# Optimization experiments

Hardware: AMD Instinct MI355X
Metric: run time of the kernel (lower is better)

## Reference

```python
import jax, jax.numpy as jnp
import numpy as np

EPS = 1e-5

@jax.custom_vjp
def spike(u):
    return (u >= 0).astype(u.dtype)

def _spike_fwd(u):
    return spike(u), u

def _spike_bwd(u, g):
    return (g / (1.0 + 5.0 * jnp.abs(u)) ** 2,)

spike.defvjp(_spike_fwd, _spike_bwd)


def setup_inputs() -> dict:
    key = jax.random.key(0)
    ks = jax.random.split(key, 20)
    B, T, IN, TH, H = 2048, 320, 64, 128, 64
    d = {}
    d['x'] = jax.random.normal(ks[0], (B, T, IN), jnp.float32)
    d['tda'] = jax.random.normal(ks[1], (B, 150), jnp.float32)
    # depthwise conv: Conv1d(64,128,k=15,pad=7,groups=64) -> kernel [128, 1, 15]
    d['conv_w'] = jax.random.normal(ks[2], (TH, 1, 15), jnp.float32) * 0.1
    d['conv_b'] = jnp.zeros((TH,), jnp.float32)
    d['bn1_g'] = jnp.ones((TH,), jnp.float32)
    d['bn1_b'] = jnp.zeros((TH,), jnp.float32)
    d['bn1_m'] = jnp.zeros((TH,), jnp.float32)
    d['bn1_v'] = jnp.ones((TH,), jnp.float32)
    # spatial_fc: Linear(128,64), init mean=0.05 std=0.1
    d['sp_w'] = 0.05 + 0.1 * jax.random.normal(ks[3], (H, TH), jnp.float32)
    d['sp_b'] = jnp.zeros((H,), jnp.float32)
    d['li_w'] = jax.random.normal(ks[4], (H, 2 * H), jnp.float32) * (1.0 / np.sqrt(2 * H))
    d['li_b'] = jnp.zeros((H,), jnp.float32)
    d['tda_w1'] = jax.random.normal(ks[5], (64, 150), jnp.float32) * (1.0 / np.sqrt(150))
    d['tda_b1'] = jnp.zeros((64,), jnp.float32)
    d['tda_w2'] = jax.random.normal(ks[6], (32, 64), jnp.float32) * 0.125
    d['tda_b2'] = jnp.zeros((32,), jnp.float32)
    dp_out = (320 // 32) * H  # 640
    d['cls_w1'] = jax.random.normal(ks[7], (128, dp_out + 32), jnp.float32) * (1.0 / np.sqrt(dp_out + 32))
    d['cls_b1'] = jnp.zeros((128,), jnp.float32)
    d['bn2_g'] = jnp.ones((128,), jnp.float32)
    d['bn2_b'] = jnp.zeros((128,), jnp.float32)
    d['bn2_m'] = jnp.zeros((128,), jnp.float32)
    d['bn2_v'] = jnp.ones((128,), jnp.float32)
    d['cls_w2'] = jax.random.normal(ks[8], (4, 128), jnp.float32) * (1.0 / np.sqrt(128))
    d['cls_b2'] = jnp.zeros((4,), jnp.float32)
    return d


def reference(x, tda, conv_w, conv_b, bn1_g, bn1_b, bn1_m, bn1_v, sp_w, sp_b,
              li_w, li_b, tda_w1, tda_b1, tda_w2, tda_b2,
              cls_w1, cls_b1, bn2_g, bn2_b, bn2_m, bn2_v, cls_w2, cls_b2):
    B, T, _ = x.shape
    L_DP, N_DP, H = 32, 16, 64
    # temp_conv (eval mode: no dropout, BN with running stats)
    xc = jnp.transpose(x, (0, 2, 1))  # [B, 64, T]
    y = jax.lax.conv_general_dilated(
        xc, conv_w, window_strides=(1,), padding=[(7, 7)],
        dimension_numbers=('NCH', 'OIH', 'NCH'), feature_group_count=64)
    y = y + conv_b[None, :, None]
    y = (y - bn1_m[None, :, None]) * jax.lax.rsqrt(bn1_v + EPS)[None, :, None] * bn1_g[None, :, None] + bn1_b[None, :, None]
    y = jax.nn.relu(y)
    y = jnp.transpose(y, (0, 2, 1))  # [B, T, 128]
    # precompute all input currents: [T, B, 64] (time-major for scan)
    cur_all = jnp.einsum('bth,oh->tbo', y, sp_w) + sp_b

    def step(carry, cur):
        mf, ms, ml = carry
        mf = 0.5 * mf + cur
        sf = spike(mf - 0.5)
        mf = mf * (1.0 - sf)
        ms = 0.9 * ms + cur
        ss = spike(ms - 1.0)
        ms = ms * (1.0 - ss)
        cur_li = jnp.concatenate([sf, ss], axis=-1) @ li_w.T + li_b
        ml = 0.9 * ml + cur_li
        return (mf, ms, ml), ml

    z0 = jnp.zeros((B, H), x.dtype)
    _, li_seq = jax.lax.scan(step, (z0, z0, z0), cur_all)  # [T, B, 64]
    li_seq = jnp.transpose(li_seq, (1, 0, 2))  # [B, T, 64]

    windows = li_seq.reshape(B, T // L_DP, L_DP, H)
    start_mean = windows[:, :, :N_DP, :].mean(axis=2)
    end_mean = windows[:, :, -N_DP:, :].mean(axis=2)
    dp_feat = (end_mean - start_mean).reshape(B, -1)  # [B, 640]

    t1 = jax.nn.relu(tda @ tda_w1.T + tda_b1)
    tda_feat = jax.nn.relu(t1 @ tda_w2.T + tda_b2)  # [B, 32]

    h = jnp.concatenate([dp_feat, tda_feat], axis=-1) @ cls_w1.T + cls_b1
    h = (h - bn2_m) * jax.lax.rsqrt(bn2_v + EPS) * bn2_g + bn2_b
    h = jax.nn.relu(h)
    return h @ cls_w2.T + cls_b2  # [B, 4]
```

## Files before the change

### kernel.cpp

```cpp
#include <hip/hip_runtime.h>

#define NT 256

#define WS_SPWT    0
#define WS_SC1     8192
#define WS_SH1     8320
#define WS_SC2     8448
#define WS_SH2     8576
#define WS_LIWT    8704
#define WS_TW1T    16896
#define WS_TW2T    26496
#define WS_CW1T    28544
#define WS_TOTAL   114560
#define WS_WG      114560
#define WS_WBASE   114688
#define WS_CURBASE (114688 + 2048*1280)
#define CUR_STRIDE 20480

__global__ void prep_kernel(
    const float* __restrict__ conv_b, const float* __restrict__ bn1_g,
    const float* __restrict__ bn1_b,  const float* __restrict__ bn1_m,
    const float* __restrict__ bn1_v,  const float* __restrict__ sp_w,
    const float* __restrict__ li_w,   const float* __restrict__ tda_w1,
    const float* __restrict__ tda_w2, const float* __restrict__ cls_w1,
    const float* __restrict__ bn2_g,  const float* __restrict__ bn2_b,
    const float* __restrict__ bn2_m,  const float* __restrict__ bn2_v,
    float* __restrict__ ws)
{
    int i = blockIdx.x * NT + threadIdx.x;
    if (i > WS_TOTAL) return;
    if (i == WS_TOTAL) {
        float g = 0.f, sE = 0.f, sL = 0.f; int w = 0;
        for (int t = 0; t < 320; ++t) {
            g = fmaf(0.9f, g, 1.f);
            int pos = t & 31;
            if (pos < 16) sE += g; else sL += g;
            if (pos == 31) { ws[WS_WG + w] = sL - sE; ++w; sE = 0.f; sL = 0.f; }
        }
        return;
    }
    if (i < WS_SC1) {
        int c = i >> 6, h = i & 63;
        ws[i] = sp_w[h*128 + c];
    } else if (i < WS_SH1) {
        int c = i - WS_SC1;
        float vv = bn1_v[c] + 1e-5f;
        ws[i] = (float)((double)bn1_g[c] / sqrt((double)vv));
    } else if (i < WS_SC2) {
        int c = i - WS_SH1;
        float vv = bn1_v[c] + 1e-5f;
        double s = (double)bn1_g[c] / sqrt((double)vv);
        ws[i] = (float)(((double)conv_b[c] - (double)bn1_m[c])*s + (double)bn1_b[c]);
    } else if (i < WS_SH2) {
        int c = i - WS_SC2;
        float vv = bn2_v[c] + 1e-5f;
        ws[i] = (float)((double)bn2_g[c] / sqrt((double)vv));
    } else if (i < WS_LIWT) {
        int c = i - WS_SH2;
        float vv = bn2_v[c] + 1e-5f;
        double s = (double)bn2_g[c] / sqrt((double)vv);
        ws[i] = (float)((double)bn2_b[c] - (double)bn2_m[c]*s);
    } else if (i < WS_TW1T) {
        int t = i - WS_LIWT; int j = t >> 6, o = t & 63;
        ws[i] = li_w[o*128 + j];
    } else if (i < WS_TW2T) {
        int t = i - WS_TW1T; int r = t >> 6, o = t & 63;
        ws[i] = tda_w1[o*150 + r];
    } else if (i < WS_CW1T) {
        int t = i - WS_TW2T; int j = t >> 5, o = t & 31;
        ws[i] = tda_w2[o*64 + j];
    } else {
        int t = i - WS_CW1T; int j = t >> 7, c = t & 127;
        ws[i] = cls_w1[c*672 + j];
    }
}

__launch_bounds__(NT, 3)
__global__ void convproj_kernel(
    const float* __restrict__ x, const float* __restrict__ conv_w,
    const float* __restrict__ ws, float* __restrict__ cur, int b0)
{
    __shared__ float smem[13312];
    float* x_lds = smem;
    float* y_lds = smem + 4992;

    const int tid  = threadIdx.x;
    const int bi   = blockIdx.x / 5;
    const int chk  = blockIdx.x % 5;
    const int b    = b0 + bi;
    const int lane = tid & 63;
    const int t0   = chk * 64;

    const int cc   = tid & 127;
    const int half = tid >> 7;
    float cwr[15];
    #pragma unroll
    for (int k = 0; k < 15; ++k) cwr[k] = conv_w[cc*15 + k];
    const float sc1 = ws[WS_SC1 + cc];
    const float sh1 = ws[WS_SH1 + cc];

    const int h0 = __builtin_amdgcn_readfirstlane((tid >> 6) << 4);
    const float* __restrict__ spwT = ws;
    const float* xb = x + (size_t)b * 20480;

    for (int idx = tid; idx < 78*16; idx += NT) {
        int trow = idx >> 4, icq = idx & 15;
        int t = t0 - 7 + trow;
        float4 v = make_float4(0.f, 0.f, 0.f, 0.f);
        if (t >= 0 && t < 320)
            v = *reinterpret_cast<const float4*>(xb + t*64 + icq*4);
        *reinterpret_cast<float4*>(&x_lds[trow*64 + icq*4]) = v;
    }
    __syncthreads();
    {
        float xr[46];
        #pragma unroll
        for (int r = 0; r < 46; ++r)
            xr[r] = x_lds[(half*32 + r)*64 + (cc >> 1)];
        #pragma unroll
        for (int i = 0; i < 32; ++i) {
            float acc = 0.f;
            #pragma unroll
            for (int k = 0; k < 15; ++k)
                acc = fmaf(xr[i + k], cwr[k], acc);
            y_lds[cc*65 + half*32 + i] = fmaxf(fmaf(acc, sc1, sh1), 0.f);
        }
    }
    __syncthreads();
    {
        float acc[16];
        #pragma unroll
        for (int j = 0; j < 16; ++j) acc[j] = 0.f;
        #pragma unroll 4
        for (int c = 0; c < 128; ++c) {
            float yv = y_lds[c*65 + lane];
            const float4* wp = reinterpret_cast<const float4*>(spwT + c*64 + h0);
            float4 w0 = wp[0], w1 = wp[1], w2 = wp[2], w3 = wp[3];
            acc[0]  = fmaf(yv, w0.x, acc[0]);
            acc[1]  = fmaf(yv, w0.y, acc[1]);
            acc[2]  = fmaf(yv, w0.z, acc[2]);
            acc[3]  = fmaf(yv, w0.w, acc[3]);
            acc[4]  = fmaf(yv, w1.x, acc[4]);
            acc[5]  = fmaf(yv, w1.y, acc[5]);
            acc[6]  = fmaf(yv, w1.z, acc[6]);
            acc[7]  = fmaf(yv, w1.w, acc[7]);
            acc[8]  = fmaf(yv, w2.x, acc[8]);
            acc[9]  = fmaf(yv, w2.y, acc[9]);
            acc[10] = fmaf(yv, w2.z, acc[10]);
            acc[11] = fmaf(yv, w2.w, acc[11]);
            acc[12] = fmaf(yv, w3.x, acc[12]);
            acc[13] = fmaf(yv, w3.y, acc[13]);
            acc[14] = fmaf(yv, w3.z, acc[14]);
            acc[15] = fmaf(yv, w3.w, acc[15]);
        }
        float* cb = cur + (size_t)bi * CUR_STRIDE + (size_t)h0 * 320 + t0 + lane;
        #pragma unroll
        for (int j = 0; j < 16; ++j)
            cb[j*320] = acc[j];
    }
}

__global__ void scan_kernel(const float* __restrict__ cur,
                            const float* __restrict__ sp_b,
                            float* __restrict__ W, int b0, int nb)
{
    const int wv = (int)((blockIdx.x * (unsigned)blockDim.x + threadIdx.x) >> 6);
    if (wv >= nb) return;
    const int lane = threadIdx.x & 63;
    const float* cb = cur + (size_t)wv * CUR_STRIDE + (size_t)lane * 320;
    const float spb = sp_b[lane];
    float* Wb = W + (size_t)(b0 + wv) * 1280;

    float mf = 0.f, ms = 0.f, rlo = 0.f, rhi = 0.f;
    float4 n0 = *reinterpret_cast<const float4*>(cb);
    float4 n1 = *reinterpret_cast<const float4*>(cb + 4);
    float4 n2 = *reinterpret_cast<const float4*>(cb + 8);
    float4 n3 = *reinterpret_cast<const float4*>(cb + 12);
    float sE_lo = 0.f, sE_hi = 0.f;

    #pragma unroll 1
    for (int tb = 0; tb < 20; ++tb) {
        float v[16];
        v[0]=n0.x; v[1]=n0.y; v[2]=n0.z; v[3]=n0.w;
        v[4]=n1.x; v[5]=n1.y; v[6]=n1.z; v[7]=n1.w;
        v[8]=n2.x; v[9]=n2.y; v[10]=n2.z; v[11]=n2.w;
        v[12]=n3.x; v[13]=n3.y; v[14]=n3.z; v[15]=n3.w;
        if (tb < 19) {
            const float* p = cb + (tb + 1) * 16;
            n0 = *reinterpret_cast<const float4*>(p);
            n1 = *reinterpret_cast<const float4*>(p + 4);
            n2 = *reinterpret_cast<const float4*>(p + 8);
            n3 = *reinterpret_cast<const float4*>(p + 12);
        }
        float slo = 0.f, shi = 0.f;
        #pragma unroll
        for (int q = 0; q < 16; ++q) {
            float c = v[q] + spb;
            mf = fmaf(0.5f, mf, c);
            bool sf = (mf - 0.5f) >= 0.f;
            ms = fmaf(0.9f, ms, c);
            bool ss = (ms - 1.0f) >= 0.f;
            mf = sf ? 0.f : mf;
            ms = ss ? 0.f : ms;
            rlo = fmaf(0.9f, rlo, sf ? 1.f : 0.f);
            rhi = fmaf(0.9f, rhi, ss ? 1.f : 0.f);
            slo += rlo; shi += rhi;
        }
        if ((tb & 1) == 0) {
            sE_lo = slo; sE_hi = shi;
        } else {
            int w = tb >> 1;
            Wb[w*128 + lane]      = slo - sE_lo;
            Wb[w*128 + 64 + lane] = shi - sE_hi;
        }
    }
}

__global__ void epilogue_kernel(
    const float* __restrict__ tda,    const float* __restrict__ li_b,
    const float* __restrict__ tda_b1, const float* __restrict__ tda_b2,
    const float* __restrict__ cls_b1, const float* __restrict__ cls_w2,
    const float* __restrict__ cls_b2, const float* __restrict__ ws,
    const float* __restrict__ W,      float* __restrict__ out)
{
    __shared__ float Wl[1280];
    __shared__ float t1[64], tf[32], dp[640], h1[128];
    const int b = blockIdx.x, tid = threadIdx.x;

    for (int i = tid; i < 1280; i += NT)
        Wl[i] = W[(size_t)b*1280 + i];
    __syncthreads();

    const float* __restrict__ liwT = ws + WS_LIWT;
    const float* __restrict__ tw1T = ws + WS_TW1T;
    const float* __restrict__ tw2T = ws + WS_TW2T;
    const float* __restrict__ cw1T = ws + WS_CW1T;
    const float* tdab = tda + b*150;

    if (tid < 64) {
        float acc = tda_b1[tid];
        for (int i2 = 0; i2 < 150; ++i2)
            acc = fmaf(tdab[i2], tw1T[i2*64 + tid], acc);
        t1[tid] = fmaxf(acc, 0.f);
    }
    __syncthreads();
    if (tid < 32) {
        float acc = tda_b2[tid];
        #pragma unroll 8
        for (int j = 0; j < 64; ++j)
            acc = fmaf(t1[j], tw2T[j*32 + tid], acc);
        tf[tid] = fmaxf(acc, 0.f);
    }
    {
        int o = tid & 63;
        for (int w = tid >> 6; w < 10; w += 4) {
            float acc = li_b[o] * ws[WS_WG + w];
            #pragma unroll 4
            for (int j = 0; j < 128; ++j)
                acc = fmaf(Wl[w*128 + j], liwT[j*64 + o], acc);
            dp[w*64 + o] = 0.0625f * acc;
        }
    }
    __syncthreads();
    if (tid < 128) {
        float acc = cls_b1[tid];
        for (int j = 0; j < 640; ++j)
            acc = fmaf(dp[j], cw1T[j*128 + tid], acc);
        #pragma unroll 4
        for (int j = 0; j < 32; ++j)
            acc = fmaf(tf[j], cw1T[(640 + j)*128 + tid], acc);
        float s2 = ws[WS_SC2 + tid], sh2 = ws[WS_SH2 + tid];
        h1[tid] = fmaxf(fmaf(acc, s2, sh2), 0.f);
    }
    __syncthreads();
    if (tid < 4) {
        float acc = cls_b2[tid];
        for (int c = 0; c < 128; ++c)
            acc = fmaf(h1[c], cls_w2[tid*128 + c], acc);
        out[b*4 + tid] = acc;
    }
}

extern "C" void kernel_launch(void* const* d_in, const int* in_sizes, int n_in,
                              void* d_out, int out_size, void* d_ws, size_t ws_size,
                              hipStream_t stream) {
    const float* x      = (const float*)d_in[0];
    const float* tda    = (const float*)d_in[1];
    const float* conv_w = (const float*)d_in[2];
    const float* conv_b = (const float*)d_in[3];
    const float* bn1_g  = (const float*)d_in[4];
    const float* bn1_b  = (const float*)d_in[5];
    const float* bn1_m  = (const float*)d_in[6];
    const float* bn1_v  = (const float*)d_in[7];
    const float* sp_w   = (const float*)d_in[8];
    const float* sp_b   = (const float*)d_in[9];
    const float* li_w   = (const float*)d_in[10];
    const float* li_b   = (const float*)d_in[11];
    const float* tda_w1 = (const float*)d_in[12];
    const float* tda_b1 = (const float*)d_in[13];
    const float* tda_w2 = (const float*)d_in[14];
    const float* tda_b2 = (const float*)d_in[15];
    const float* cls_w1 = (const float*)d_in[16];
    const float* cls_b1 = (const float*)d_in[17];
    const float* bn2_g  = (const float*)d_in[18];
    const float* bn2_b  = (const float*)d_in[19];
    const float* bn2_m  = (const float*)d_in[20];
    const float* bn2_v  = (const float*)d_in[21];
    const float* cls_w2 = (const float*)d_in[22];
    const float* cls_b2 = (const float*)d_in[23];
    float* ws  = (float*)d_ws;
    float* out = (float*)d_out;

    const int B = in_sizes[0] / (320 * 64);

    prep_kernel<<<(WS_TOTAL + 1 + NT - 1)/NT, NT, 0, stream>>>(
        conv_b, bn1_g, bn1_b, bn1_m, bn1_v, sp_w,
        li_w, tda_w1, tda_w2, cls_w1,
        bn2_g, bn2_b, bn2_m, bn2_v, ws);

    long cap = (long)(ws_size / 4) - (long)WS_CURBASE;
    int nbg = (int)(cap / CUR_STRIDE);
    if (nbg < 1) nbg = 1;
    if (nbg > B) nbg = B;

    for (int g0 = 0; g0 < B; g0 += nbg) {
        int nb = (B - g0 < nbg) ? (B - g0) : nbg;
        convproj_kernel<<<nb*5, NT, 0, stream>>>(
            x, conv_w, ws, ws + WS_CURBASE, g0);
        scan_kernel<<<(nb + 3)/4, NT, 0, stream>>>(
            ws + WS_CURBASE, sp_b, ws + WS_WBASE, g0, nb);
    }

    epilogue_kernel<<<B, NT, 0, stream>>>(
        tda, li_b, tda_b1, tda_b2, cls_b1, cls_w2, cls_b2,
        ws, ws + WS_WBASE, out);
}
```

Before: 292.9 us.

## Compute spatial projection with split-bf16 MFMA instead of scalar FMA

Replaces the scalar FP32 128x64 spatial projection in the conv kernel with bf16 MFMA 16x16x32 instructions. Both the weights and the conv activations are split into high and low bf16 parts, and three MFMAs per k-step approximate FP32 precision. Activations are stored in LDS as swizzled bf16 hi/lo planes, and the prep kernel writes the split weights. This moves the main FMA work onto matrix cores, at the cost of extra conversions and some precision risk from dropping the lo*lo term.

```diff
diff --git a/kernel.cpp b/kernel.cpp
--- a/kernel.cpp
+++ b/kernel.cpp
@@ -2,7 +2,18 @@
 
 #define NT 256
 
-#define WS_SPWT    0
+typedef __attribute__((ext_vector_type(8))) short short8b;
+typedef __attribute__((ext_vector_type(4))) float f32x4;
+
+__device__ inline unsigned short f2bf(float f) {
+    unsigned u = __float_as_uint(f);
+    unsigned r = (u + 0x7fffu + ((u >> 16) & 1u)) >> 16;
+    return (unsigned short)r;
+}
+__device__ inline float bf2f(unsigned short h) {
+    return __uint_as_float(((unsigned)h) << 16);
+}
+
 #define WS_SC1     8192
 #define WS_SH1     8320
 #define WS_SC2     8448
@@ -39,9 +50,13 @@
         }
         return;
     }
-    if (i < WS_SC1) {
-        int c = i >> 6, h = i & 63;
-        ws[i] = sp_w[h*128 + c];
+    if (i < 8192) {
+        unsigned short* ws16 = (unsigned short*)ws;
+        float v = sp_w[i];
+        unsigned short hv = f2bf(v);
+        ws16[i] = hv;
+        ws16[8192 + i] = f2bf(v - bf2f(hv));
+    } else if (i < WS_SC1) {
     } else if (i < WS_SH1) {
         int c = i - WS_SC1;
         float vv = bn1_v[c] + 1e-5f;
@@ -80,28 +95,17 @@
     const float* __restrict__ x, const float* __restrict__ conv_w,
     const float* __restrict__ ws, float* __restrict__ cur, int b0)
 {
-    __shared__ float smem[13312];
+    __shared__ float smem[13184];
     float* x_lds = smem;
-    float* y_lds = smem + 4992;
-
-    const int tid  = threadIdx.x;
-    const int bi   = blockIdx.x / 5;
-    const int chk  = blockIdx.x % 5;
-    const int b    = b0 + bi;
-    const int lane = tid & 63;
-    const int t0   = chk * 64;
-
-    const int cc   = tid & 127;
-    const int half = tid >> 7;
-    float cwr[15];
-    #pragma unroll
-    for (int k = 0; k < 15; ++k) cwr[k] = conv_w[cc*15 + k];
-    const float sc1 = ws[WS_SC1 + cc];
-    const float sh1 = ws[WS_SH1 + cc];
-
-    const int h0 = __builtin_amdgcn_readfirstlane((tid >> 6) << 4);
-    const float* __restrict__ spwT = ws;
-    const float* xb = x + (size_t)b * 20480;
+    unsigned short* yh = (unsigned short*)(smem + 4992);
+    unsigned short* yl = yh + 8192;
+
+    const int tid = threadIdx.x;
+    const int bi  = blockIdx.x / 5;
+    const int chk = blockIdx.x % 5;
+    const int t0  = chk * 64;
+
+    const float* xb = x + (size_t)(b0 + bi) * 20480;
 
     for (int idx = tid; idx < 78*16; idx += NT) {
         int trow = idx >> 4, icq = idx & 15;
@@ -111,7 +115,16 @@
             v = *reinterpret_cast<const float4*>(xb + t*64 + icq*4);
         *reinterpret_cast<float4*>(&x_lds[trow*64 + icq*4]) = v;
     }
-    __syncthreads();
+
+    const int cc = tid & 127, half = tid >> 7;
+    float cwr[15];
+    #pragma unroll
+    for (int k = 0; k < 15; ++k) cwr[k] = conv_w[cc*15 + k];
+    const float sc1 = ws[WS_SC1 + cc];
+    const float sh1 = ws[WS_SH1 + cc];
+
+    __syncthreads();
+
     {
         float xr[46];
         #pragma unroll
@@ -119,44 +132,58 @@
             xr[r] = x_lds[(half*32 + r)*64 + (cc >> 1)];
         #pragma unroll
         for (int i = 0; i < 32; ++i) {
-            float acc = 0.f;
+            float a = 0.f;
             #pragma unroll
             for (int k = 0; k < 15; ++k)
-                acc = fmaf(xr[i + k], cwr[k], acc);
-            y_lds[cc*65 + half*32 + i] = fmaxf(fmaf(acc, sc1, sh1), 0.f);
-        }
-    }
-    __syncthreads();
+                a = fmaf(xr[i + k], cwr[k], a);
+            float yv = fmaxf(fmaf(a, sc1, sh1), 0.f);
+            int t = half*32 + i;
+            unsigned off = (unsigned)(t*256) + (((unsigned)(cc*2)) ^ ((unsigned)((t & 7) << 4)));
+            unsigned short hv = f2bf(yv);
+            *(unsigned short*)((char*)yh + off) = hv;
+            *(unsigned short*)((char*)yl + off) = f2bf(yv - bf2f(hv));
+        }
+    }
+    __syncthreads();
+
     {
-        float acc[16];
-        #pragma unroll
-        for (int j = 0; j < 16; ++j) acc[j] = 0.f;
-        #pragma unroll 4
-        for (int c = 0; c < 128; ++c) {
-            float yv = y_lds[c*65 + lane];
-            const float4* wp = reinterpret_cast<const float4*>(spwT + c*64 + h0);
-            float4 w0 = wp[0], w1 = wp[1], w2 = wp[2], w3 = wp[3];
-            acc[0]  = fmaf(yv, w0.x, acc[0]);
-            acc[1]  = fmaf(yv, w0.y, acc[1]);
-            acc[2]  = fmaf(yv, w0.z, acc[2]);
-            acc[3]  = fmaf(yv, w0.w, acc[3]);
-            acc[4]  = fmaf(yv, w1.x, acc[4]);
-            acc[5]  = fmaf(yv, w1.y, acc[5]);
-            acc[6]  = fmaf(yv, w1.z, acc[6]);
-            acc[7]  = fmaf(yv, w1.w, acc[7]);
-            acc[8]  = fmaf(yv, w2.x, acc[8]);
-            acc[9]  = fmaf(yv, w2.y, acc[9]);
-            acc[10] = fmaf(yv, w2.z, acc[10]);
-            acc[11] = fmaf(yv, w2.w, acc[11]);
-            acc[12] = fmaf(yv, w3.x, acc[12]);
-            acc[13] = fmaf(yv, w3.y, acc[13]);
-            acc[14] = fmaf(yv, w3.z, acc[14]);
-            acc[15] = fmaf(yv, w3.w, acc[15]);
-        }
-        float* cb = cur + (size_t)bi * CUR_STRIDE + (size_t)h0 * 320 + t0 + lane;
-        #pragma unroll
-        for (int j = 0; j < 16; ++j)
-            cb[j*320] = acc[j];
+        const int l  = tid & 63;
+        const int nt = tid >> 6;
+        const int tl = nt*16 + (l & 15);
+        const int kg = l >> 4;
+
+        short8b Bh[4], Bl[4];
+        const unsigned tswz = (unsigned)((tl & 7) << 4);
+        #pragma unroll
+        for (int ks = 0; ks < 4; ++ks) {
+            unsigned off = (unsigned)(tl*256) + (((unsigned)(ks*64 + kg*16)) ^ tswz);
+            Bh[ks] = *(const short8b*)((const char*)yh + off);
+            Bl[ks] = *(const short8b*)((const char*)yl + off);
+        }
+
+        const unsigned short* wsh = (const unsigned short*)ws;
+        const unsigned short* wsl = wsh + 8192;
+        const int ha = l & 15;
+        float* cb0 = cur + (size_t)bi * CUR_STRIDE + (size_t)(kg*4)*320 + t0 + tl;
+
+        #pragma unroll
+        for (int mt = 0; mt < 4; ++mt) {
+            const unsigned short* ap = wsh + (mt*16 + ha)*128;
+            const unsigned short* lp = wsl + (mt*16 + ha)*128;
+            f32x4 acc = {0.f, 0.f, 0.f, 0.f};
+            #pragma unroll
+            for (int ks = 0; ks < 4; ++ks) {
+                short8b Ah = *(const short8b*)(ap + ks*32 + kg*8);
+                short8b Al = *(const short8b*)(lp + ks*32 + kg*8);
+                acc = __builtin_amdgcn_mfma_f32_16x16x32_bf16(Ah, Bh[ks], acc, 0, 0, 0);
+                acc = __builtin_amdgcn_mfma_f32_16x16x32_bf16(Ah, Bl[ks], acc, 0, 0, 0);
+                acc = __builtin_amdgcn_mfma_f32_16x16x32_bf16(Al, Bh[ks], acc, 0, 0, 0);
+            }
+            float* cb = cb0 + (size_t)(mt*16)*320;
+            #pragma unroll
+            for (int r = 0; r < 4; ++r)
+                cb[(size_t)r*320] = acc[r];
+        }
     }
 }
 
```

Measured after the change: 321.3 us. 9.7% more time.

## Rework conv/projection with swizzled LDS, packed FMA, and deeper scan prefetch

Applied to the files above, without the earlier changes.

The convolution stage now loads x directly from global memory into registers, with each thread computing both output channels of one input channel. This removes the x staging buffer in LDS and shrinks shared memory, which allows an occupancy bound of 4 blocks. The conv output is stored as channel pairs in an XOR-swizzled LDS layout, and the projection uses v_pk_fma_f32 with scalar weight pairs to halve the FMA instruction count. The scan kernel prefetches two 16-step blocks ahead instead of one, at the cost of more registers and strided uncoalesced global loads of x.

```diff
diff --git a/kernel.cpp b/kernel.cpp
--- a/kernel.cpp
+++ b/kernel.cpp
@@ -2,7 +2,9 @@
 
 #define NT 256
 
-#define WS_SPWT    0
+typedef __attribute__((ext_vector_type(2))) float f32x2;
+
+#define WS_SPWP    0
 #define WS_SC1     8192
 #define WS_SH1     8320
 #define WS_SC2     8448
@@ -40,8 +42,9 @@
         return;
     }
     if (i < WS_SC1) {
-        int c = i >> 6, h = i & 63;
-        ws[i] = sp_w[h*128 + c];
+        int p = i >> 1, e = i & 1;
+        int c2 = p >> 6, h = p & 63;
+        ws[i] = sp_w[h*128 + 2*c2 + e];
     } else if (i < WS_SH1) {
         int c = i - WS_SC1;
         float vv = bn1_v[c] + 1e-5f;
@@ -75,88 +78,101 @@
     }
 }
 
-__launch_bounds__(NT, 3)
+__launch_bounds__(NT, 4)
 __global__ void convproj_kernel(
     const float* __restrict__ x, const float* __restrict__ conv_w,
     const float* __restrict__ ws, float* __restrict__ cur, int b0)
 {
-    __shared__ float smem[13312];
-    float* x_lds = smem;
-    float* y_lds = smem + 4992;
-
-    const int tid  = threadIdx.x;
-    const int bi   = blockIdx.x / 5;
-    const int chk  = blockIdx.x % 5;
-    const int b    = b0 + bi;
-    const int lane = tid & 63;
-    const int t0   = chk * 64;
-
-    const int cc   = tid & 127;
-    const int half = tid >> 7;
-    float cwr[15];
+    __shared__ float y_lds[64*128];
+
+    const int tid = threadIdx.x;
+    const int bi  = blockIdx.x / 5;
+    const int chk = blockIdx.x % 5;
+    const int t0  = chk * 64;
+    const int ic  = tid & 63;
+    const int tg  = tid >> 6;
+
+    float w0[15], w1[15];
     #pragma unroll
-    for (int k = 0; k < 15; ++k) cwr[k] = conv_w[cc*15 + k];
-    const float sc1 = ws[WS_SC1 + cc];
-    const float sh1 = ws[WS_SH1 + cc];
-
-    const int h0 = __builtin_amdgcn_readfirstlane((tid >> 6) << 4);
-    const float* __restrict__ spwT = ws;
-    const float* xb = x + (size_t)b * 20480;
-
-    for (int idx = tid; idx < 78*16; idx += NT) {
-        int trow = idx >> 4, icq = idx & 15;
-        int t = t0 - 7 + trow;
-        float4 v = make_float4(0.f, 0.f, 0.f, 0.f);
-        if (t >= 0 && t < 320)
-            v = *reinterpret_cast<const float4*>(xb + t*64 + icq*4);
-        *reinterpret_cast<float4*>(&x_lds[trow*64 + icq*4]) = v;
-    }
-    __syncthreads();
+    for (int k = 0; k < 15; ++k) {
+        w0[k] = conv_w[(2*ic)*15 + k];
+        w1[k] = conv_w[(2*ic + 1)*15 + k];
+    }
+    const float sA = ws[WS_SC1 + 2*ic],     hA = ws[WS_SH1 + 2*ic];
+    const float sB = ws[WS_SC1 + 2*ic + 1], hB = ws[WS_SH1 + 2*ic + 1];
+
+    const float* xb = x + (size_t)(b0 + bi) * 20480 + ic;
+    float xr[30];
+    #pragma unroll
+    for (int r = 0; r < 30; ++r) {
+        int t = t0 + tg*16 - 7 + r;
+        xr[r] = ((unsigned)t < 320u) ? xb[(size_t)t * 64] : 0.f;
+    }
+
+    char* yb = (char*)y_lds;
+    #pragma unroll
+    for (int j = 0; j < 16; ++j) {
+        float a0 = 0.f, a1 = 0.f;
+        #pragma unroll
+        for (int k = 0; k < 15; ++k) {
+            a0 = fmaf(xr[j + k], w0[k], a0);
+            a1 = fmaf(xr[j + k], w1[k], a1);
+        }
+        float y0 = fmaxf(fmaf(a0, sA, hA), 0.f);
+        float y1 = fmaxf(fmaf(a1, sB, hB), 0.f);
+        int tt = tg*16 + j;
+        unsigned off = (unsigned)(tt*512) + (((unsigned)(ic*8)) ^ ((unsigned)((tt & 15) << 3)));
+        *reinterpret_cast<f32x2*>(yb + off) = f32x2{y0, y1};
+    }
+    __syncthreads();
+
     {
-        float xr[46];
+        const int lane = tid & 63;
+        const int h0 = __builtin_amdgcn_readfirstlane((tid >> 6) << 4);
+        const f32x2* __restrict__ wp = reinterpret_cast<const f32x2*>(ws);
+
+        f32x2 acc[16];
         #pragma unroll
-        for (int r = 0; r < 46; ++r)
-            xr[r] = x_lds[(half*32 + r)*64 + (cc >> 1)];
-        #pragma unroll
-        for (int i = 0; i < 32; ++i) {
-            float acc = 0.f;
+        for (int j = 0; j < 16; ++j) acc[j] = f32x2{0.f, 0.f};
+
+        const unsigned tb  = (unsigned)(lane * 512);
+        const unsigned tsw = (unsigned)((lane & 15) << 3);
+        #pragma unroll 4
+        for (int c2 = 0; c2 < 64; ++c2) {
+            f32x2 y2 = *reinterpret_cast<const f32x2*>(yb + (tb + (((unsigned)(c2*8)) ^ tsw)));
+            const f32x2* wrow = wp + c2*64 + h0;
             #pragma unroll
-            for (int k = 0; k < 15; ++k)
-                acc = fmaf(xr[i + k], cwr[k], acc);
-            y_lds[cc*65 + half*32 + i] = fmaxf(fmaf(acc, sc1, sh1), 0.f);
-        }
-    }
-    __syncthreads();
-    {
-        float acc[16];
-        #pragma unroll
-        for (int j = 0; j < 16; ++j) acc[j] = 0.f;
-        #pragma unroll 4
-        for (int c = 0; c < 128; ++c) {
-            float yv = y_lds[c*65 + lane];
-            const float4* wp = reinterpret_cast<const float4*>(spwT + c*64 + h0);
-            float4 w0 = wp[0], w1 = wp[1], w2 = wp[2], w3 = wp[3];
-            acc[0]  = fmaf(yv, w0.x, acc[0]);
-            acc[1]  = fmaf(yv, w0.y, acc[1]);
-            acc[2]  = fmaf(yv, w0.z, acc[2]);
-            acc[3]  = fmaf(yv, w0.w, acc[3]);
-            acc[4]  = fmaf(yv, w1.x, acc[4]);
-            acc[5]  = fmaf(yv, w1.y, acc[5]);
-            acc[6]  = fmaf(yv, w1.z, acc[6]);
-            acc[7]  = fmaf(yv, w1.w, acc[7]);
-            acc[8]  = fmaf(yv, w2.x, acc[8]);
-            acc[9]  = fmaf(yv, w2.y, acc[9]);
-            acc[10] = fmaf(yv, w2.z, acc[10]);
-            acc[11] = fmaf(yv, w2.w, acc[11]);
-            acc[12] = fmaf(yv, w3.x, acc[12]);
-            acc[13] = fmaf(yv, w3.y, acc[13]);
-            acc[14] = fmaf(yv, w3.z, acc[14]);
-            acc[15] = fmaf(yv, w3.w, acc[15]);
+            for (int j = 0; j < 16; ++j) {
+                asm("v_pk_fma_f32 %0, %1, %2, %0"
+                    : "+v"(acc[j]) : "v"(y2), "s"(wrow[j]));
+            }
         }
         float* cb = cur + (size_t)bi * CUR_STRIDE + (size_t)h0 * 320 + t0 + lane;
         #pragma unroll
         for (int j = 0; j < 16; ++j)
-            cb[j*320] = acc[j];
+            cb[(size_t)j*320] = acc[j].x + acc[j].y;
+    }
+}
+
+__device__ __forceinline__ void lif16(float4 n0, float4 n1, float4 n2, float4 n3,
+    float spb, float& mf, float& ms, float& rlo, float& rhi,
+    float& slo, float& shi)
+{
+    float v[16] = {n0.x,n0.y,n0.z,n0.w, n1.x,n1.y,n1.z,n1.w,
+                   n2.x,n2.y,n2.z,n2.w, n3.x,n3.y,n3.z,n3.w};
+    slo = 0.f; shi = 0.f;
+    #pragma unroll
+    for (int q = 0; q < 16; ++q) {
+        float c = v[q] + spb;
+        mf = fmaf(0.5f, mf, c);
+        bool sf = (mf - 0.5f) >= 0.f;
+        ms = fmaf(0.9f, ms, c);
+        bool ss = (ms - 1.0f) >= 0.f;
+        mf = sf ? 0.f : mf;
+        ms = ss ? 0.f : ms;
+        rlo = fmaf(0.9f, rlo, sf ? 1.f : 0.f);
+        rhi = fmaf(0.9f, rhi, ss ? 1.f : 0.f);
+        slo += rlo; shi += rhi;
     }
 }
 
@@ -172,47 +188,38 @@
     float* Wb = W + (size_t)(b0 + wv) * 1280;
 
     float mf = 0.f, ms = 0.f, rlo = 0.f, rhi = 0.f;
-    float4 n0 = *reinterpret_cast<const float4*>(cb);
-    float4 n1 = *reinterpret_cast<const float4*>(cb + 4);
-    float4 n2 = *reinterpret_cast<const float4*>(cb + 8);
-    float4 n3 = *reinterpret_cast<const float4*>(cb + 12);
-    float sE_lo = 0.f, sE_hi = 0.f;
+
+    float4 A0 = *reinterpret_cast<const float4*>(cb);
+    float4 A1 = *reinterpret_cast<const float4*>(cb + 4);
+    float4 A2 = *reinterpret_cast<const float4*>(cb + 8);
+    float4 A3 = *reinterpret_cast<const float4*>(cb + 12);
+    float4 B0 = *reinterpret_cast<const float4*>(cb + 16);
+    float4 B1 = *reinterpret_cast<const float4*>(cb + 20);
+    float4 B2 = *reinterpret_cast<const float4*>(cb + 24);
+    float4 B3 = *reinterpret_cast<const float4*>(cb + 28);
 
     #pragma unroll 1
-    for (int tb = 0; tb < 20; ++tb) {
-        float v[16];
-        v[0]=n0.x; v[1]=n0.y; v[2]=n0.z; v[3]=n0.w;
-        v[4]=n1.x; v[5]=n1.y; v[6]=n1.z; v[7]=n1.w;
-        v[8]=n2.x; v[9]=n2.y; v[10]=n2.z; v[11]=n2.w;
-        v[12]=n3.x; v[13]=n3.y; v[14]=n3.z; v[15]=n3.w;
-        if (tb < 19) {
-            const float* p = cb + (tb + 1) * 16;
-            n0 = *reinterpret_cast<const float4*>(p);
-            n1 = *reinterpret_cast<const float4*>(p + 4);
-            n2 = *reinterpret_cast<const float4*>(p + 8);
-            n3 = *reinterpret_cast<const float4*>(p + 12);
-        }
-        float slo = 0.f, shi = 0.f;
-        #pragma unroll
-        for (int q = 0; q < 16; ++q) {
-            float c = v[q] + spb;
-            mf = fmaf(0.5f, mf, c);
-            bool sf = (mf - 0.5f) >= 0.f;
-            ms = fmaf(0.9f, ms, c);
-            bool ss = (ms - 1.0f) >= 0.f;
-            mf = sf ? 0.f : mf;
-            ms = ss ? 0.f : ms;
-            rlo = fmaf(0.9f, rlo, sf ? 1.f : 0.f);
-            rhi = fmaf(0.9f, rhi, ss ? 1.f : 0.f);
-            slo += rlo; shi += rhi;
-        }
-        if ((tb & 1) == 0) {
-            sE_lo = slo; sE_hi = shi;
-        } else {
-            int w = tb >> 1;
-            Wb[w*128 + lane]      = slo - sE_lo;
-            Wb[w*128 + 64 + lane] = shi - sE_hi;
-        }
+    for (int tb = 0; tb < 20; tb += 2) {
+        float sE_lo, sE_hi, slo, shi;
+        lif16(A0, A1, A2, A3, spb, mf, ms, rlo, rhi, sE_lo, sE_hi);
+        if (tb + 2 < 20) {
+            const float* p = cb + (tb + 2) * 16;
+            A0 = *reinterpret_cast<const float4*>(p);
+            A1 = *reinterpret_cast<const float4*>(p + 4);
+            A2 = *reinterpret_cast<const float4*>(p + 8);
+            A3 = *reinterpret_cast<const float4*>(p + 12);
+        }
+        lif16(B0, B1, B2, B3, spb, mf, ms, rlo, rhi, slo, shi);
+        if (tb + 3 < 20) {
+            const float* p = cb + (tb + 3) * 16;
+            B0 = *reinterpret_cast<const float4*>(p);
+            B1 = *reinterpret_cast<const float4*>(p + 4);
+            B2 = *reinterpret_cast<const float4*>(p + 8);
+            B3 = *reinterpret_cast<const float4*>(p + 12);
+        }
+        int wdx = tb >> 1;
+        Wb[wdx*128 + lane]      = slo - sE_lo;
+        Wb[wdx*128 + 64 + lane] = shi - sE_hi;
     }
 }
 
```

Result: slower. 495.9 us (+69.3%).
